# Performance work log

Hardware: AMD Instinct MI355X
Metric: run time of the kernel (lower is better)

## Reference

```python
import jax, jax.numpy as jnp
import numpy as np

NUM_LAYERS = 6
D = 16           # physical_dim == bond_dim (required for multi-layer consistency)
B, S, FIN = 128, 2048, 128


def setup_inputs() -> dict:
    key = jax.random.key(0)
    k0, k1, k2, k3 = jax.random.split(key, 4)
    return {
        "sequence": jax.random.normal(k0, (B, S, FIN), jnp.float32),
        "W_emb": jax.random.normal(k1, (FIN, D), jnp.float32) * 0.05,
        "b_emb": jnp.zeros((D,), jnp.float32),
        "u": jax.random.normal(k2, (NUM_LAYERS, D, D, D, D), jnp.float32) * 0.1,
        "w": jax.random.normal(k3, (NUM_LAYERS, D, D, D), jnp.float32) * 0.1,
    }


def _ent_entropy(sA, sB):
    # sA: (B, pA, d), sB: (B, pB, d)
    corr = jnp.einsum('bik,bjk->bij', sA, sB)          # (B, pA, pB)
    s = jnp.linalg.svd(corr, compute_uv=False)          # (B, min(pA,pB))
    sn = s / (jnp.sum(s, axis=1, keepdims=True) + 1e-8)
    return -jnp.sum(sn * jnp.log(sn + 1e-8), axis=1)    # (B,)


def _phi_q(sites):
    # sites: (B, n, d), n >= 4 and even
    n = sites.shape[1]
    mid = n // 2
    S_int = _ent_entropy(sites[:, :mid], sites[:, mid:])
    A, Bp = sites[:, :mid], sites[:, mid:]
    S1 = _ent_entropy(A[:, :mid // 2], A[:, mid // 2:])
    S2 = _ent_entropy(Bp[:, :(n - mid) // 2], Bp[:, (n - mid) // 2:])
    return jnp.maximum(S_int - (S1 + S2), 0.0)


def _apply_layer(sites, u_l, w_l):
    # sites: (B, n, d) with n even. Disentangle adjacent pairs, then coarse-grain.
    b, n, d = sites.shape
    s = sites.reshape(b, n // 2, 2, d)
    # disentangler: einsum('ijkl,bi,bj->bkl') batched over pairs p
    comb = jnp.einsum('ijkl,bpi,bpj->bpkl', u_l, s[:, :, 0], s[:, :, 1])
    o1 = comb.mean(axis=3)   # mean over l -> (b, p, k)
    o2 = comb.mean(axis=2)   # mean over k -> (b, p, l)
    # isometry acts on consecutive disentangled pairs (o1_i, o2_i)
    return jnp.einsum('aij,bpi,bpj->bpa', w_l, o1, o2)  # (b, n//2, bond)


def reference(sequence, W_emb, b_emb, u, w):
    emb = sequence @ W_emb + b_emb                       # (B, S, D)
    norm = jnp.linalg.norm(emb, axis=-1, keepdims=True)
    sites = emb / jnp.maximum(norm, 1e-12)               # F.normalize(dim=-1)
    for l in range(NUM_LAYERS):
        sites = _apply_layer(sites, u[l], w[l])
    phi_q = _phi_q(sites)
    return sites, phi_q
```

## Files before the change

kernel.cpp:

```cpp
#include <hip/hip_runtime.h>
#include <hip/hip_bf16.h>
#include <math.h>

#define BATCH 128
#define SEQ   2048
#define FIN   128
#define DD    16
#define NLAYERS 6
#define SST   20

#define BUFA_F  (BATCH*SEQ*DD)
#define BUFB_F  (BATCH*(SEQ/2)*DD)
#define COEF_OFF (BUFA_F + BUFB_F)
#define ENT_OFF  (COEF_OFF + NLAYERS*12288)

__global__ __launch_bounds__(256) void k_prep(const float* __restrict__ u,
                                              const float* __restrict__ w,
                                              float* __restrict__ coef) {
    int l  = blockIdx.x;
    int ij = threadIdx.x;
    const float* ub = u + (size_t)l*65536 + (size_t)ij*256;
    float a1[16], a2[16];
#pragma unroll
    for (int k = 0; k < 16; ++k) { a1[k] = 0.0f; a2[k] = 0.0f; }
#pragma unroll
    for (int k = 0; k < 16; ++k) {
#pragma unroll
        for (int z = 0; z < 16; ++z) {
            float v = ub[k*16 + z];
            a1[k] += v;
            a2[z] += v;
        }
    }
    float* ucb = coef + (size_t)l*12288 + ij*32;
#pragma unroll
    for (int k = 0; k < 16; ++k) {
        ucb[k]      = a1[k]*(1.0f/16.0f);
        ucb[16 + k] = a2[k]*(1.0f/16.0f);
    }
    const float* wb = w + (size_t)l*4096;
    float* wtb = coef + (size_t)l*12288 + 8192 + ij*16;
#pragma unroll
    for (int a = 0; a < 16; ++a) wtb[a] = wb[a*256 + ij];
}

__global__ __launch_bounds__(256) void k_embed(const float* __restrict__ seq,
                                               const float* __restrict__ W,
                                               const float* __restrict__ bias,
                                               float* __restrict__ out) {
    __shared__ float wl[2048];
    int t = threadIdx.x;
    for (int x = t; x < 2048; x += 256) wl[x] = W[x];
    int q = t & 3;
    size_t row = ((size_t)blockIdx.x*256 + t) >> 2;
    float acc[4];
    {
        float4 bv = *(const float4*)(bias + q*4);
        acc[0] = bv.x; acc[1] = bv.y; acc[2] = bv.z; acc[3] = bv.w;
    }
    __syncthreads();

    const float4* rp = (const float4*)seq + row*32;
#pragma unroll 8
    for (int kk = 0; kk < 32; ++kk) {
        float4 rv = rp[kk];
        float rc[4] = { rv.x, rv.y, rv.z, rv.w };
#pragma unroll
        for (int c = 0; c < 4; ++c) {
            float4 wv = *(const float4*)&wl[(kk*4 + c)*16 + q*4];
            float s = rc[c];
            acc[0] = fmaf(s, wv.x, acc[0]);
            acc[1] = fmaf(s, wv.y, acc[1]);
            acc[2] = fmaf(s, wv.z, acc[2]);
            acc[3] = fmaf(s, wv.w, acc[3]);
        }
    }
    float p = 0.0f;
#pragma unroll
    for (int j = 0; j < 4; ++j) p = fmaf(acc[j], acc[j], p);
    p += __shfl_xor(p, 1);
    p += __shfl_xor(p, 2);
    float inv = 1.0f / fmaxf(sqrtf(p), 1e-12f);
    *(float4*)(out + row*16 + q*4) = make_float4(acc[0]*inv, acc[1]*inv,
                                                 acc[2]*inv, acc[3]*inv);
}

__global__ __launch_bounds__(256) void k_layer(const float* __restrict__ in,
                                               float* __restrict__ outp,
                                               const float* __restrict__ coefl) {
    __shared__ float cbuf[8192];
    __shared__ float spl[64*36];
    int t = threadIdx.x;
    int og = t & 7, pg = t >> 3;
    int lane = t & 63, base = lane & ~7;

    const float4* wtf = (const float4*)(coefl + 8192);
    float4 wr0 = wtf[0*256 + t];
    float4 wr1 = wtf[1*256 + t];
    float4 wr2 = wtf[2*256 + t];
    float4 wr3 = wtf[3*256 + t];

    {
        const float4* ucf = (const float4*)coefl;
        float4* c4 = (float4*)cbuf;
#pragma unroll
        for (int it = 0; it < 8; ++it) c4[it*256 + t] = ucf[it*256 + t];
    }
    {
        const float4* ing = (const float4*)in + (size_t)blockIdx.x*512;
        float4 v0 = ing[t];
        float4 v1 = ing[t + 256];
        *(float4*)&spl[(t >> 3)*36 + (t & 7)*4]        = v0;
        *(float4*)&spl[((t >> 3) + 32)*36 + (t & 7)*4] = v1;
    }
    __syncthreads();

    float s1v[2][16];
#pragma unroll
    for (int pp = 0; pp < 2; ++pp) {
        int p = pg + pp*32;
#pragma unroll
        for (int g = 0; g < 4; ++g) {
            float4 v = *(const float4*)&spl[p*36 + 16 + g*4];
            s1v[pp][g*4+0]=v.x; s1v[pp][g*4+1]=v.y; s1v[pp][g*4+2]=v.z; s1v[pp][g*4+3]=v.w;
        }
    }

    float accv[2][4];
    accv[0][0]=0.f; accv[0][1]=0.f; accv[0][2]=0.f; accv[0][3]=0.f;
    accv[1][0]=0.f; accv[1][1]=0.f; accv[1][2]=0.f; accv[1][3]=0.f;

    for (int i = 0; i < 16; ++i) {
        float s0a = spl[pg*36 + i];
        float s0b = spl[(pg + 32)*36 + i];
        const float4* uc = (const float4*)&cbuf[i*512] + og;
#pragma unroll
        for (int j = 0; j < 16; ++j) {
            float4 cv = uc[j*8];
            float pa = s0a * s1v[0][j];
            float pb = s0b * s1v[1][j];
            accv[0][0] = fmaf(pa, cv.x, accv[0][0]);
            accv[0][1] = fmaf(pa, cv.y, accv[0][1]);
            accv[0][2] = fmaf(pa, cv.z, accv[0][2]);
            accv[0][3] = fmaf(pa, cv.w, accv[0][3]);
            accv[1][0] = fmaf(pb, cv.x, accv[1][0]);
            accv[1][1] = fmaf(pb, cv.y, accv[1][1]);
            accv[1][2] = fmaf(pb, cv.z, accv[1][2]);
            accv[1][3] = fmaf(pb, cv.w, accv[1][3]);
        }
    }
    __syncthreads();
    {
        float4* c4 = (float4*)cbuf;
        c4[0*256 + t] = wr0;
        c4[1*256 + t] = wr1;
        c4[2*256 + t] = wr2;
        c4[3*256 + t] = wr3;
    }
    __syncthreads();

    float o2f[2][16];
#pragma unroll
    for (int j = 0; j < 16; ++j) {
        int src = base + 4 + (j >> 2);
        o2f[0][j] = __shfl(accv[0][j & 3], src, 64);
        o2f[1][j] = __shfl(accv[1][j & 3], src, 64);
    }

    float r0a = 0.f, r1a = 0.f, r0b = 0.f, r1b = 0.f;
    for (int grp = 0; grp < 4; ++grp) {
#pragma unroll
        for (int c = 0; c < 4; ++c) {
            float o1a = __shfl(accv[0][c], base + grp, 64);
            float o1b = __shfl(accv[1][c], base + grp, 64);
            const float2* wrow = (const float2*)&cbuf[(grp*4 + c)*256] + og;
#pragma unroll
            for (int j = 0; j < 16; ++j) {
                float2 wv = wrow[j*8];
                float qa = o1a * o2f[0][j];
                float qb = o1b * o2f[1][j];
                r0a = fmaf(qa, wv.x, r0a);
                r1a = fmaf(qa, wv.y, r1a);
                r0b = fmaf(qb, wv.x, r0b);
                r1b = fmaf(qb, wv.y, r1b);
            }
        }
    }

    size_t gp = (size_t)blockIdx.x*64;
    *(float2*)&outp[(gp + pg)*16 + og*2]      = make_float2(r0a, r1a);
    *(float2*)&outp[(gp + pg + 32)*16 + og*2] = make_float2(r0b, r1b);
}

template<int P, bool LAST>
__device__ __forceinline__ void layer_body(float* sL, const float* coef,
                                           float* outp, int npg, int t, int bid) {
    int og = t & 7, pg = t >> 3;
    int lane = t & 63, base = lane & ~7;
    bool act = pg < npg;

    float accv[P][4];
    float s1v[P][16];
#pragma unroll
    for (int pp = 0; pp < P; ++pp) { accv[pp][0]=0.f; accv[pp][1]=0.f; accv[pp][2]=0.f; accv[pp][3]=0.f; }

    if (act) {
#pragma unroll
        for (int pp = 0; pp < P; ++pp) {
            int r = 2*(pg + pp*32) + 1;
#pragma unroll
            for (int g = 0; g < 4; ++g) {
                float4 v = *(const float4*)&sL[r*SST + g*4];
                s1v[pp][g*4+0]=v.x; s1v[pp][g*4+1]=v.y; s1v[pp][g*4+2]=v.z; s1v[pp][g*4+3]=v.w;
            }
        }
        for (int i = 0; i < 16; ++i) {
            float s0[P];
#pragma unroll
            for (int pp = 0; pp < P; ++pp) s0[pp] = sL[(2*(pg + pp*32))*SST + i];
            const float4* uc = (const float4*)&coef[i*512] + og;
#pragma unroll
            for (int j = 0; j < 16; ++j) {
                float4 cv = uc[j*8];
#pragma unroll
                for (int pp = 0; pp < P; ++pp) {
                    float p = s0[pp] * s1v[pp][j];
                    accv[pp][0] = fmaf(p, cv.x, accv[pp][0]);
                    accv[pp][1] = fmaf(p, cv.y, accv[pp][1]);
                    accv[pp][2] = fmaf(p, cv.z, accv[pp][2]);
                    accv[pp][3] = fmaf(p, cv.w, accv[pp][3]);
                }
            }
        }
    }
    __syncthreads();

    if (act) {
        float o2f[P][16];
#pragma unroll
        for (int j = 0; j < 16; ++j) {
            int src = base + 4 + (j >> 2);
#pragma unroll
            for (int pp = 0; pp < P; ++pp)
                o2f[pp][j] = __shfl(accv[pp][j & 3], src, 64);
        }
        float r0[P], r1[P];
#pragma unroll
        for (int pp = 0; pp < P; ++pp) { r0[pp] = 0.f; r1[pp] = 0.f; }
        for (int grp = 0; grp < 4; ++grp) {
#pragma unroll
            for (int c = 0; c < 4; ++c) {
                float o1i[P];
#pragma unroll
                for (int pp = 0; pp < P; ++pp)
                    o1i[pp] = __shfl(accv[pp][c], base + grp, 64);
#pragma unroll
                for (int j = 0; j < 16; ++j) {
                    float2 wv = *(const float2*)&coef[8192 + ((grp*4+c)*16 + j)*16 + og*2];
#pragma unroll
                    for (int pp = 0; pp < P; ++pp) {
                        float q = o1i[pp] * o2f[pp][j];
                        r0[pp] = fmaf(q, wv.x, r0[pp]);
                        r1[pp] = fmaf(q, wv.y, r1[pp]);
                    }
                }
            }
        }
        if (LAST) {
#pragma unroll
            for (int pp = 0; pp < P; ++pp) {
                int p = pg + pp*32;
                *(float2*)&outp[((size_t)bid*32 + p)*16 + og*2] = make_float2(r0[pp], r1[pp]);
            }
        } else {
#pragma unroll
            for (int pp = 0; pp < P; ++pp) {
                int p = pg + pp*32;
                *(float2*)&sL[p*SST + og*2] = make_float2(r0[pp], r1[pp]);
            }
        }
    }
    __syncthreads();
}

__global__ __launch_bounds__(256) void k_tail(const float* __restrict__ in,
                                              const float* __restrict__ coefg,
                                              float* __restrict__ outp) {
    __shared__ float coef[12288];
    __shared__ float sL[256*SST];
    int t = threadIdx.x, bid = blockIdx.x;

    const float4* in4 = (const float4*)in + (size_t)bid*1024;
#pragma unroll
    for (int it = 0; it < 4; ++it) {
        int f = it*256 + t;
        *(float4*)&sL[(f >> 2)*SST + (f & 3)*4] = in4[f];
    }
#pragma unroll 1
    for (int l = 0; l < 3; ++l) {
        const float4* src = (const float4*)(coefg + (size_t)(3 + l)*12288);
        __syncthreads();
        for (int x = t; x < 3072; x += 256) ((float4*)coef)[x] = src[x];
        __syncthreads();
        switch (l) {
            case 0: layer_body<4,false>(sL, coef, outp, 32, t, bid); break;
            case 1: layer_body<2,false>(sL, coef, outp, 32, t, bid); break;
            case 2: layer_body<1,true >(sL, coef, outp, 32, t, bid); break;
        }
    }
}

__device__ __forceinline__ void rot_cs(float al, float be, float ga, float& c, float& s) {
    float ze = (be - al) / (2.0f * ga);
    float tt = copysignf(1.0f, ze) / (fabsf(ze) + sqrtf(1.0f + ze*ze));
    c = 1.0f / sqrtf(1.0f + tt*tt);
    s = c * tt;
}

__global__ __launch_bounds__(64) void k_phi(const float* __restrict__ sites,
                                            float* __restrict__ ent) {
    __shared__ float S[512];
    __shared__ float C[256];
    __shared__ float sv[16];
    int bid = blockIdx.x;
    int role = bid >> 7;
    int b = bid & 127;
    int t = threadIdx.x;
    const float* sp = sites + (size_t)b*512;

    if (role == 0) {
        for (int x = t; x < 512; x += 64) S[x] = sp[x];
        __syncthreads();
        for (int e = t; e < 256; e += 64) {
            int i = e & 15, j = e >> 4;
            float a = 0.0f;
            for (int k = 0; k < 16; ++k) a = fmaf(S[i*16+k], S[(16+j)*16+k], a);
            C[j*16 + i] = a;
        }
        __syncthreads();
        for (int sw = 0; sw < 12; ++sw) {
            for (int r = 0; r < 15; ++r) {
                int pr = t >> 3, sub = t & 7;
                int p, q;
                if (pr == 0) { p = 15; q = r; }
                else { p = (r + pr) % 15; q = (r + 15 - pr) % 15; }
                float u0 = C[p*16 + 2*sub],   u1v = C[p*16 + 2*sub + 1];
                float v0 = C[q*16 + 2*sub],   v1v = C[q*16 + 2*sub + 1];
                float al = u0*u0 + u1v*u1v;
                float be = v0*v0 + v1v*v1v;
                float ga = u0*v0 + u1v*v1v;
                al += __shfl_xor(al,1); al += __shfl_xor(al,2); al += __shfl_xor(al,4);
                be += __shfl_xor(be,1); be += __shfl_xor(be,2); be += __shfl_xor(be,4);
                ga += __shfl_xor(ga,1); ga += __shfl_xor(ga,2); ga += __shfl_xor(ga,4);
                if (ga != 0.0f) {
                    float c, s; rot_cs(al, be, ga, c, s);
                    C[p*16 + 2*sub]     = fmaf(c, u0, -s*v0);
                    C[p*16 + 2*sub + 1] = fmaf(c, u1v, -s*v1v);
                    C[q*16 + 2*sub]     = fmaf(s, u0,  c*v0);
                    C[q*16 + 2*sub + 1] = fmaf(s, u1v, c*v1v);
                }
                __syncthreads();
            }
        }
        if (t < 16) {
            float s2 = 0.0f;
            for (int rr = 0; rr < 16; ++rr) { float v = C[t*16+rr]; s2 = fmaf(v, v, s2); }
            sv[t] = sqrtf(s2);
        }
        __syncthreads();
        if (t == 0) {
            float sum = 0.0f;
            for (int i2 = 0; i2 < 16; ++i2) sum += sv[i2];
            float den = sum + 1e-8f;
            float e2 = 0.0f;
            for (int i2 = 0; i2 < 16; ++i2) {
                float sn = sv[i2] / den;
                e2 -= sn * logf(sn + 1e-8f);
            }
            ent[b] = e2;
        }
    } else {
        int ro = (role == 1) ? 0 : 256;
        for (int x = t; x < 256; x += 64) S[x] = sp[ro + x];
        __syncthreads();
        if (t < 64) {
            int i = t & 7, j = t >> 3;
            float a = 0.0f;
            for (int k = 0; k < 16; ++k) a = fmaf(S[i*16+k], S[(8+j)*16+k], a);
            C[j*8 + i] = a;
        }
        __syncthreads();
        for (int sw = 0; sw < 12; ++sw) {
            for (int r = 0; r < 7; ++r) {
                if (t < 32) {
                    int pr = t >> 3, sub = t & 7;
                    int p, q;
                    if (pr == 0) { p = 7; q = r; }
                    else { p = (r + pr) % 7; q = (r + 7 - pr) % 7; }
                    float uu = C[p*8 + sub], vv = C[q*8 + sub];
                    float al = uu*uu, be = vv*vv, ga = uu*vv;
                    al += __shfl_xor(al,1); al += __shfl_xor(al,2); al += __shfl_xor(al,4);
                    be += __shfl_xor(be,1); be += __shfl_xor(be,2); be += __shfl_xor(be,4);
                    ga += __shfl_xor(ga,1); ga += __shfl_xor(ga,2); ga += __shfl_xor(ga,4);
                    if (ga != 0.0f) {
                        float c, s; rot_cs(al, be, ga, c, s);
                        C[p*8 + sub] = fmaf(c, uu, -s*vv);
                        C[q*8 + sub] = fmaf(s, uu,  c*vv);
                    }
                }
                __syncthreads();
            }
        }
        if (t < 8) {
            float s2 = 0.0f;
            for (int rr = 0; rr < 8; ++rr) { float v = C[t*8+rr]; s2 = fmaf(v, v, s2); }
            sv[t] = sqrtf(s2);
        }
        __syncthreads();
        if (t == 0) {
            float sum = 0.0f;
            for (int i2 = 0; i2 < 8; ++i2) sum += sv[i2];
            float den = sum + 1e-8f;
            float e2 = 0.0f;
            for (int i2 = 0; i2 < 8; ++i2) {
                float sn = sv[i2] / den;
                e2 -= sn * logf(sn + 1e-8f);
            }
            ent[role*128 + b] = e2;
        }
    }
}

__global__ __launch_bounds__(128) void k_phi2(const float* __restrict__ ent,
                                              float* __restrict__ phi) {
    int b = threadIdx.x;
    phi[b] = fmaxf(ent[b] - (ent[128 + b] + ent[256 + b]), 0.0f);
}

extern "C" void kernel_launch(void* const* d_in, const int* in_sizes, int n_in,
                              void* d_out, int out_size, void* d_ws, size_t ws_size,
                              hipStream_t stream) {
    const float* seq  = (const float*)d_in[0];
    const float* W    = (const float*)d_in[1];
    const float* bias = (const float*)d_in[2];
    const float* u    = (const float*)d_in[3];
    const float* w    = (const float*)d_in[4];
    float* out = (float*)d_out;
    float* ws  = (float*)d_ws;

    float* bufA  = ws;
    float* bufB  = ws + BUFA_F;
    float* coefw = ws + COEF_OFF;
    float* entb  = ws + ENT_OFF;

    k_prep <<<NLAYERS, 256, 0, stream>>>(u, w, coefw);
    k_embed<<<(BATCH*SEQ*4)/256, 256, 0, stream>>>(seq, W, bias, bufA);

    k_layer<<<2048, 256, 0, stream>>>(bufA, bufB, coefw + 0*12288);
    k_layer<<<1024, 256, 0, stream>>>(bufB, bufA, coefw + 1*12288);
    k_layer<<< 512, 256, 0, stream>>>(bufA, bufB, coefw + 2*12288);
    k_tail <<< 128, 256, 0, stream>>>(bufB, coefw, out);

    k_phi <<<3*BATCH, 64, 0, stream>>>(out, entb);
    k_phi2<<<1, 128, 0, stream>>>(entb, out + BATCH*32*DD);
}
```

Baseline: 232.3 us.

## Fuse embedding and all six layers into one kernel; cut Jacobi sweeps

Replaces the separate embed, three per-layer kernels and tail kernel with one kernel. Each block loads 128 sequence rows, embeds and normalizes them into shared memory, then runs all six layers on-chip, so the large intermediate global buffers go away. The SVD Jacobi sweep count drops from 12 to 8, and k_prep now reads u with float4 loads. The trade-offs are idle threads in the later layers, where few pairs remain, and possibly less converged singular values from fewer sweeps.

```diff
diff --git a/kernel.cpp b/kernel.cpp
--- a/kernel.cpp
+++ b/kernel.cpp
@@ -7,29 +7,29 @@
 #define FIN   128
 #define DD    16
 #define NLAYERS 6
-#define SST   20
-
-#define BUFA_F  (BATCH*SEQ*DD)
-#define BUFB_F  (BATCH*(SEQ/2)*DD)
-#define COEF_OFF (BUFA_F + BUFB_F)
-#define ENT_OFF  (COEF_OFF + NLAYERS*12288)
+#define SST   16
+#define SWEEPS 8
+
+#define COEF_OFF 0
+#define ENT_OFF  (NLAYERS*12288)
+
 
 __global__ __launch_bounds__(256) void k_prep(const float* __restrict__ u,
                                               const float* __restrict__ w,
                                               float* __restrict__ coef) {
     int l  = blockIdx.x;
     int ij = threadIdx.x;
-    const float* ub = u + (size_t)l*65536 + (size_t)ij*256;
+    const float4* ub4 = (const float4*)(u + (size_t)l*65536 + (size_t)ij*256);
     float a1[16], a2[16];
 #pragma unroll
     for (int k = 0; k < 16; ++k) { a1[k] = 0.0f; a2[k] = 0.0f; }
 #pragma unroll
     for (int k = 0; k < 16; ++k) {
 #pragma unroll
-        for (int z = 0; z < 16; ++z) {
-            float v = ub[k*16 + z];
-            a1[k] += v;
-            a2[z] += v;
+        for (int z4 = 0; z4 < 4; ++z4) {
+            float4 v = ub4[k*4 + z4];
+            a1[k] += v.x + v.y + v.z + v.w;
+            a2[z4*4+0] += v.x; a2[z4*4+1] += v.y; a2[z4*4+2] += v.z; a2[z4*4+3] += v.w;
         }
     }
     float* ucb = coef + (size_t)l*12288 + ij*32;
@@ -44,153 +44,6 @@
     for (int a = 0; a < 16; ++a) wtb[a] = wb[a*256 + ij];
 }
 
-__global__ __launch_bounds__(256) void k_embed(const float* __restrict__ seq,
-                                               const float* __restrict__ W,
-                                               const float* __restrict__ bias,
-                                               float* __restrict__ out) {
-    __shared__ float wl[2048];
-    int t = threadIdx.x;
-    for (int x = t; x < 2048; x += 256) wl[x] = W[x];
-    int q = t & 3;
-    size_t row = ((size_t)blockIdx.x*256 + t) >> 2;
-    float acc[4];
-    {
-        float4 bv = *(const float4*)(bias + q*4);
-        acc[0] = bv.x; acc[1] = bv.y; acc[2] = bv.z; acc[3] = bv.w;
-    }
-    __syncthreads();
-
-    const float4* rp = (const float4*)seq + row*32;
-#pragma unroll 8
-    for (int kk = 0; kk < 32; ++kk) {
-        float4 rv = rp[kk];
-        float rc[4] = { rv.x, rv.y, rv.z, rv.w };
-#pragma unroll
-        for (int c = 0; c < 4; ++c) {
-            float4 wv = *(const float4*)&wl[(kk*4 + c)*16 + q*4];
-            float s = rc[c];
-            acc[0] = fmaf(s, wv.x, acc[0]);
-            acc[1] = fmaf(s, wv.y, acc[1]);
-            acc[2] = fmaf(s, wv.z, acc[2]);
-            acc[3] = fmaf(s, wv.w, acc[3]);
-        }
-    }
-    float p = 0.0f;
-#pragma unroll
-    for (int j = 0; j < 4; ++j) p = fmaf(acc[j], acc[j], p);
-    p += __shfl_xor(p, 1);
-    p += __shfl_xor(p, 2);
-    float inv = 1.0f / fmaxf(sqrtf(p), 1e-12f);
-    *(float4*)(out + row*16 + q*4) = make_float4(acc[0]*inv, acc[1]*inv,
-                                                 acc[2]*inv, acc[3]*inv);
-}
-
-__global__ __launch_bounds__(256) void k_layer(const float* __restrict__ in,
-                                               float* __restrict__ outp,
-                                               const float* __restrict__ coefl) {
-    __shared__ float cbuf[8192];
-    __shared__ float spl[64*36];
-    int t = threadIdx.x;
-    int og = t & 7, pg = t >> 3;
-    int lane = t & 63, base = lane & ~7;
-
-    const float4* wtf = (const float4*)(coefl + 8192);
-    float4 wr0 = wtf[0*256 + t];
-    float4 wr1 = wtf[1*256 + t];
-    float4 wr2 = wtf[2*256 + t];
-    float4 wr3 = wtf[3*256 + t];
-
-    {
-        const float4* ucf = (const float4*)coefl;
-        float4* c4 = (float4*)cbuf;
-#pragma unroll
-        for (int it = 0; it < 8; ++it) c4[it*256 + t] = ucf[it*256 + t];
-    }
-    {
-        const float4* ing = (const float4*)in + (size_t)blockIdx.x*512;
-        float4 v0 = ing[t];
-        float4 v1 = ing[t + 256];
-        *(float4*)&spl[(t >> 3)*36 + (t & 7)*4]        = v0;
-        *(float4*)&spl[((t >> 3) + 32)*36 + (t & 7)*4] = v1;
-    }
-    __syncthreads();
-
-    float s1v[2][16];
-#pragma unroll
-    for (int pp = 0; pp < 2; ++pp) {
-        int p = pg + pp*32;
-#pragma unroll
-        for (int g = 0; g < 4; ++g) {
-            float4 v = *(const float4*)&spl[p*36 + 16 + g*4];
-            s1v[pp][g*4+0]=v.x; s1v[pp][g*4+1]=v.y; s1v[pp][g*4+2]=v.z; s1v[pp][g*4+3]=v.w;
-        }
-    }
-
-    float accv[2][4];
-    accv[0][0]=0.f; accv[0][1]=0.f; accv[0][2]=0.f; accv[0][3]=0.f;
-    accv[1][0]=0.f; accv[1][1]=0.f; accv[1][2]=0.f; accv[1][3]=0.f;
-
-    for (int i = 0; i < 16; ++i) {
-        float s0a = spl[pg*36 + i];
-        float s0b = spl[(pg + 32)*36 + i];
-        const float4* uc = (const float4*)&cbuf[i*512] + og;
-#pragma unroll
-        for (int j = 0; j < 16; ++j) {
-            float4 cv = uc[j*8];
-            float pa = s0a * s1v[0][j];
-            float pb = s0b * s1v[1][j];
-            accv[0][0] = fmaf(pa, cv.x, accv[0][0]);
-            accv[0][1] = fmaf(pa, cv.y, accv[0][1]);
-            accv[0][2] = fmaf(pa, cv.z, accv[0][2]);
-            accv[0][3] = fmaf(pa, cv.w, accv[0][3]);
-            accv[1][0] = fmaf(pb, cv.x, accv[1][0]);
-            accv[1][1] = fmaf(pb, cv.y, accv[1][1]);
-            accv[1][2] = fmaf(pb, cv.z, accv[1][2]);
-            accv[1][3] = fmaf(pb, cv.w, accv[1][3]);
-        }
-    }
-    __syncthreads();
-    {
-        float4* c4 = (float4*)cbuf;
-        c4[0*256 + t] = wr0;
-        c4[1*256 + t] = wr1;
-        c4[2*256 + t] = wr2;
-        c4[3*256 + t] = wr3;
-    }
-    __syncthreads();
-
-    float o2f[2][16];
-#pragma unroll
-    for (int j = 0; j < 16; ++j) {
-        int src = base + 4 + (j >> 2);
-        o2f[0][j] = __shfl(accv[0][j & 3], src, 64);
-        o2f[1][j] = __shfl(accv[1][j & 3], src, 64);
-    }
-
-    float r0a = 0.f, r1a = 0.f, r0b = 0.f, r1b = 0.f;
-    for (int grp = 0; grp < 4; ++grp) {
-#pragma unroll
-        for (int c = 0; c < 4; ++c) {
-            float o1a = __shfl(accv[0][c], base + grp, 64);
-            float o1b = __shfl(accv[1][c], base + grp, 64);
-            const float2* wrow = (const float2*)&cbuf[(grp*4 + c)*256] + og;
-#pragma unroll
-            for (int j = 0; j < 16; ++j) {
-                float2 wv = wrow[j*8];
-                float qa = o1a * o2f[0][j];
-                float qb = o1b * o2f[1][j];
-                r0a = fmaf(qa, wv.x, r0a);
-                r1a = fmaf(qa, wv.y, r1a);
-                r0b = fmaf(qb, wv.x, r0b);
-                r1b = fmaf(qb, wv.y, r1b);
-            }
-        }
-    }
-
-    size_t gp = (size_t)blockIdx.x*64;
-    *(float2*)&outp[(gp + pg)*16 + og*2]      = make_float2(r0a, r1a);
-    *(float2*)&outp[(gp + pg + 32)*16 + og*2] = make_float2(r0b, r1b);
-}
 
 template<int P, bool LAST>
 __device__ __forceinline__ void layer_body(float* sL, const float* coef,
@@ -234,79 +87,180 @@
         }
     }
     __syncthreads();
-
-    if (act) {
-        float o2f[P][16];
-#pragma unroll
-        for (int j = 0; j < 16; ++j) {
-            int src = base + 4 + (j >> 2);
-#pragma unroll
-            for (int pp = 0; pp < P; ++pp)
-                o2f[pp][j] = __shfl(accv[pp][j & 3], src, 64);
-        }
-        float r0[P], r1[P];
-#pragma unroll
-        for (int pp = 0; pp < P; ++pp) { r0[pp] = 0.f; r1[pp] = 0.f; }
-        for (int grp = 0; grp < 4; ++grp) {
+    return_from_phase1: ;
+}
+
+
+__global__ __launch_bounds__(256, 4) void k_fused(const float* __restrict__ seq,
+                                                  const float* __restrict__ W,
+                                                  const float* __restrict__ bias,
+                                                  const float* __restrict__ coefg,
+                                                  float* __restrict__ outp) {
+    __shared__ float pool[10240];
+    float* sL   = pool;
+    float* cbuf = pool + 2048;
+    float* sW   = pool + 2048;
+    float* sR   = pool + 4096;
+    int t = threadIdx.x;
+    int bid = blockIdx.x;
+    int og = t & 7, pg = t >> 3;
+    int lane = t & 63, base = lane & ~7;
+
+    for (int x = t; x < 2048; x += 256) sW[x] = W[x];
+    int q = t & 7, lr = t >> 3;
+    float2 bv = *(const float2*)(bias + 2*q);
+#pragma unroll 1
+    for (int ps = 0; ps < 4; ++ps) {
+        const float4* seq4 = (const float4*)seq + ((size_t)bid*128 + ps*32)*32;
+#pragma unroll
+        for (int it = 0; it < 4; ++it) {
+            int idx = t + it*256;
+            *(float4*)&sR[(idx >> 5)*132 + (idx & 31)*4] = seq4[idx];
+        }
+        __syncthreads();
+        float acc0 = bv.x, acc1 = bv.y;
+#pragma unroll 8
+        for (int kk = 0; kk < 32; ++kk) {
+            float4 rv = *(const float4*)&sR[lr*132 + kk*4];
+            float rc[4] = { rv.x, rv.y, rv.z, rv.w };
 #pragma unroll
             for (int c = 0; c < 4; ++c) {
-                float o1i[P];
-#pragma unroll
-                for (int pp = 0; pp < P; ++pp)
-                    o1i[pp] = __shfl(accv[pp][c], base + grp, 64);
-#pragma unroll
-                for (int j = 0; j < 16; ++j) {
-                    float2 wv = *(const float2*)&coef[8192 + ((grp*4+c)*16 + j)*16 + og*2];
-#pragma unroll
-                    for (int pp = 0; pp < P; ++pp) {
-                        float q = o1i[pp] * o2f[pp][j];
-                        r0[pp] = fmaf(q, wv.x, r0[pp]);
-                        r1[pp] = fmaf(q, wv.y, r1[pp]);
+                float2 wv = *(const float2*)&sW[(kk*4 + c)*16 + 2*q];
+                acc0 = fmaf(rc[c], wv.x, acc0);
+                acc1 = fmaf(rc[c], wv.y, acc1);
+            }
+        }
+        float p = fmaf(acc0, acc0, acc1*acc1);
+        p += __shfl_xor(p, 1);
+        p += __shfl_xor(p, 2);
+        p += __shfl_xor(p, 4);
+        float inv = 1.0f / fmaxf(sqrtf(p), 1e-12f);
+        *(float2*)&sL[(ps*32 + lr)*SST + 2*q] = make_float2(acc0*inv, acc1*inv);
+        __syncthreads();
+    }
+
+#pragma unroll 1
+    for (int l = 0; l < NLAYERS; ++l) {
+        const float* coefl = coefg + (size_t)l*12288;
+        const float4* wtf = (const float4*)(coefl + 8192);
+        float4 wr0 = wtf[0*256 + t];
+        float4 wr1 = wtf[1*256 + t];
+        float4 wr2 = wtf[2*256 + t];
+        float4 wr3 = wtf[3*256 + t];
+        {
+            const float4* ucf = (const float4*)coefl;
+            float4* c4 = (float4*)cbuf;
+#pragma unroll
+            for (int it = 0; it < 8; ++it) c4[it*256 + t] = ucf[it*256 + t];
+        }
+        __syncthreads();
+
+        int npairs = 64 >> l;
+        int npg = npairs > 32 ? 32 : npairs;
+        int P = npairs > 32 ? 2 : 1;
+        bool act = pg < npg;
+
+        float accv[2][4];
+        accv[0][0]=0.f; accv[0][1]=0.f; accv[0][2]=0.f; accv[0][3]=0.f;
+        accv[1][0]=0.f; accv[1][1]=0.f; accv[1][2]=0.f; accv[1][3]=0.f;
+        float s1v[2][16];
+
+        if (act) {
+#pragma unroll
+            for (int pp = 0; pp < 2; ++pp) {
+                int r = 2*(pg + pp*32) + 1;
+                if (pp < P) {
+#pragma unroll
+                    for (int g = 0; g < 4; ++g) {
+                        float4 v = *(const float4*)&sL[r*SST + g*4];
+                        s1v[pp][g*4+0]=v.x; s1v[pp][g*4+1]=v.y; s1v[pp][g*4+2]=v.z; s1v[pp][g*4+3]=v.w;
                     }
                 }
             }
-        }
-        if (LAST) {
-#pragma unroll
-            for (int pp = 0; pp < P; ++pp) {
-                int p = pg + pp*32;
-                *(float2*)&outp[((size_t)bid*32 + p)*16 + og*2] = make_float2(r0[pp], r1[pp]);
-            }
-        } else {
-#pragma unroll
-            for (int pp = 0; pp < P; ++pp) {
-                int p = pg + pp*32;
-                *(float2*)&sL[p*SST + og*2] = make_float2(r0[pp], r1[pp]);
-            }
-        }
-    }
-    __syncthreads();
-}
-
-__global__ __launch_bounds__(256) void k_tail(const float* __restrict__ in,
-                                              const float* __restrict__ coefg,
-                                              float* __restrict__ outp) {
-    __shared__ float coef[12288];
-    __shared__ float sL[256*SST];
-    int t = threadIdx.x, bid = blockIdx.x;
-
-    const float4* in4 = (const float4*)in + (size_t)bid*1024;
-#pragma unroll
-    for (int it = 0; it < 4; ++it) {
-        int f = it*256 + t;
-        *(float4*)&sL[(f >> 2)*SST + (f & 3)*4] = in4[f];
-    }
-#pragma unroll 1
-    for (int l = 0; l < 3; ++l) {
-        const float4* src = (const float4*)(coefg + (size_t)(3 + l)*12288);
-        __syncthreads();
-        for (int x = t; x < 3072; x += 256) ((float4*)coef)[x] = src[x];
-        __syncthreads();
-        switch (l) {
-            case 0: layer_body<4,false>(sL, coef, outp, 32, t, bid); break;
-            case 1: layer_body<2,false>(sL, coef, outp, 32, t, bid); break;
-            case 2: layer_body<1,true >(sL, coef, outp, 32, t, bid); break;
-        }
+            if (P == 2) {
+                for (int i = 0; i < 16; ++i) {
+                    float s0a = sL[(2*pg)*SST + i];
+                    float s0b = sL[(2*(pg+32))*SST + i];
+                    const float4* uc = (const float4*)&cbuf[i*512] + og;
+#pragma unroll
+                    for (int j = 0; j < 16; ++j) {
+                        float4 cv = uc[j*8];
+                        float pa = s0a * s1v[0][j];
+                        float pb = s0b * s1v[1][j];
+                        accv[0][0] = fmaf(pa, cv.x, accv[0][0]);
+                        accv[0][1] = fmaf(pa, cv.y, accv[0][1]);
+                        accv[0][2] = fmaf(pa, cv.z, accv[0][2]);
+                        accv[0][3] = fmaf(pa, cv.w, accv[0][3]);
+                        accv[1][0] = fmaf(pb, cv.x, accv[1][0]);
+                        accv[1][1] = fmaf(pb, cv.y, accv[1][1]);
+                        accv[1][2] = fmaf(pb, cv.z, accv[1][2]);
+                        accv[1][3] = fmaf(pb, cv.w, accv[1][3]);
+                    }
+                }
+            } else {
+                for (int i = 0; i < 16; ++i) {
+                    float s0a = sL[(2*pg)*SST + i];
+                    const float4* uc = (const float4*)&cbuf[i*512] + og;
+#pragma unroll
+                    for (int j = 0; j < 16; ++j) {
+                        float4 cv = uc[j*8];
+                        float pa = s0a * s1v[0][j];
+                        accv[0][0] = fmaf(pa, cv.x, accv[0][0]);
+                        accv[0][1] = fmaf(pa, cv.y, accv[0][1]);
+                        accv[0][2] = fmaf(pa, cv.z, accv[0][2]);
+                        accv[0][3] = fmaf(pa, cv.w, accv[0][3]);
+                    }
+                }
+            }
+        }
+        __syncthreads();
+        {
+            float4* c4 = (float4*)cbuf;
+            c4[0*256 + t] = wr0;
+            c4[1*256 + t] = wr1;
+            c4[2*256 + t] = wr2;
+            c4[3*256 + t] = wr3;
+        }
+        __syncthreads();
+
+        if (act) {
+            float o2f[2][16];
+#pragma unroll
+            for (int j = 0; j < 16; ++j) {
+                int src = base + 4 + (j >> 2);
+                o2f[0][j] = __shfl(accv[0][j & 3], src, 64);
+                o2f[1][j] = __shfl(accv[1][j & 3], src, 64);
+            }
+            float r0a = 0.f, r1a = 0.f, r0b = 0.f, r1b = 0.f;
+            for (int grp = 0; grp < 4; ++grp) {
+#pragma unroll
+                for (int c = 0; c < 4; ++c) {
+                    float o1a = __shfl(accv[0][c], base + grp, 64);
+                    float o1b = __shfl(accv[1][c], base + grp, 64);
+                    const float2* wrow = (const float2*)&cbuf[(grp*4 + c)*256] + og;
+#pragma unroll
+                    for (int j = 0; j < 16; ++j) {
+                        float2 wv = wrow[j*8];
+                        float qa = o1a * o2f[0][j];
+                        r0a = fmaf(qa, wv.x, r0a);
+                        r1a = fmaf(qa, wv.y, r1a);
+                        if (P == 2) {
+                            float qb = o1b * o2f[1][j];
+                            r0b = fmaf(qb, wv.x, r0b);
+                            r1b = fmaf(qb, wv.y, r1b);
+                        }
+                    }
+                }
+            }
+            if (l == NLAYERS - 1) {
+                *(float2*)&outp[((size_t)bid*2 + pg)*16 + og*2] = make_float2(r0a, r1a);
+            } else {
+                *(float2*)&sL[pg*SST + og*2] = make_float2(r0a, r1a);
+                if (P == 2)
+                    *(float2*)&sL[(pg+32)*SST + og*2] = make_float2(r0b, r1b);
+            }
+        }
+        __syncthreads();
     }
 }
 
@@ -338,7 +292,7 @@
             C[j*16 + i] = a;
         }
         __syncthreads();
-        for (int sw = 0; sw < 12; ++sw) {
+        for (int sw = 0; sw < SWEEPS; ++sw) {
             for (int r = 0; r < 15; ++r) {
                 int pr = t >> 3, sub = t & 7;
                 int p, q;
@@ -390,7 +344,7 @@
             C[j*8 + i] = a;
         }
         __syncthreads();
-        for (int sw = 0; sw < 12; ++sw) {
+        for (int sw = 0; sw < SWEEPS; ++sw) {
             for (int r = 0; r < 7; ++r) {
                 if (t < 32) {
                     int pr = t >> 3, sub = t & 7;
@@ -448,19 +402,11 @@
     float* out = (float*)d_out;
     float* ws  = (float*)d_ws;
 
-    float* bufA  = ws;
-    float* bufB  = ws + BUFA_F;
     float* coefw = ws + COEF_OFF;
     float* entb  = ws + ENT_OFF;
 
     k_prep <<<NLAYERS, 256, 0, stream>>>(u, w, coefw);
-    k_embed<<<(BATCH*SEQ*4)/256, 256, 0, stream>>>(seq, W, bias, bufA);
-
-    k_layer<<<2048, 256, 0, stream>>>(bufA, bufB, coefw + 0*12288);
-    k_layer<<<1024, 256, 0, stream>>>(bufB, bufA, coefw + 1*12288);
-    k_layer<<< 512, 256, 0, stream>>>(bufA, bufB, coefw + 2*12288);
-    k_tail <<< 128, 256, 0, stream>>>(bufB, coefw, out);
-
-    k_phi <<<3*BATCH, 64, 0, stream>>>(out, entb);
-    k_phi2<<<1, 128, 0, stream>>>(entb, out + BATCH*32*DD);
-}
+    k_fused<<<(BATCH*SEQ)/128, 256, 0, stream>>>(seq, W, bias, coefw, out);
+    k_phi  <<<3*BATCH, 64, 0, stream>>>(out, entb);
+    k_phi2 <<<1, 128, 0, stream>>>(entb, out + BATCH*32*DD);
+}
```

After: 294.3 us. 26.7% more time.
